# Kernel optimization log

Hardware: AMD Instinct MI355X
Metric: run time of the kernel (lower is better)

The kernel has to match this reference:

```python
import jax, jax.numpy as jnp
import numpy as np

D = 120000   # sample_size
H1 = 600     # sample_size/200
H2 = 300     # sample_size/400
H3 = 200     # sample_size/600
DENSITY = 0.1  # sparselinear default connectivity
B = 512
EPS = 1e-5

_LAYER_SPECS = [(H1, D), (H1, H1), (H2, H1), (H3, H2), (H3, H3)]


def _make_idx(key, out_d, in_d, nnz):
    k1, k2 = jax.random.split(key)
    rows = jax.random.randint(k1, (nnz,), 0, out_d)
    cols = jax.random.randint(k2, (nnz,), 0, in_d)
    return jnp.stack([rows, cols]).astype(jnp.int32)


def setup_inputs() -> dict:
    key = jax.random.key(0)
    ks = jax.random.split(key, 32)
    inp = {"x": jax.random.normal(ks[0], (B, D), jnp.float32)}
    for i, (o, ii) in enumerate(_LAYER_SPECS, 1):
        nnz = int(DENSITY * o * ii)
        scale = 1.0 / np.sqrt(DENSITY * ii)  # kaiming-like fan-in scaling on nonzeros
        inp[f"idx{i}"] = _make_idx(ks[3 * i], o, ii, nnz)
        inp[f"val{i}"] = jax.random.normal(ks[3 * i + 1], (nnz,), jnp.float32) * scale
        inp[f"b{i}"] = jnp.zeros((o,), jnp.float32)
    for j, d in enumerate([H1, H2, H3], 1):
        inp[f"g{j}"] = jnp.ones((d,), jnp.float32)
        inp[f"be{j}"] = jnp.zeros((d,), jnp.float32)
    return inp


def _sp_linear(x, idx, vals, bias, out_d):
    # COO sparse linear: y = x @ W^T + b, W scattered from (row, col, val)
    in_d = x.shape[1]
    W = jnp.zeros((out_d, in_d), x.dtype).at[idx[0], idx[1]].add(vals)
    return x @ W.T + bias


def _bn(x, g, b):
    # BatchNorm1d, training mode: biased batch variance
    m = x.mean(axis=0)
    v = x.var(axis=0)
    return (x - m) * jax.lax.rsqrt(v + EPS) * g + b


def reference(x, idx1, val1, b1, idx2, val2, b2, idx3, val3, b3,
              idx4, val4, b4, idx5, val5, b5,
              g1, be1, g2, be2, g3, be3):
    h = jax.nn.silu(_bn(_sp_linear(x, idx1, val1, b1, H1), g1, be1))
    h = jax.nn.silu(_sp_linear(h, idx2, val2, b2, H1))
    h = jax.nn.silu(_bn(_sp_linear(h, idx3, val3, b3, H2), g2, be2))
    h = jax.nn.silu(_bn(_sp_linear(h, idx4, val4, b4, H3), g3, be3))
    return _sp_linear(h, idx5, val5, b5, H3)
```

## Files before the change

kernel.cpp:

```cpp
#include <hip/hip_runtime.h>

typedef unsigned short ushort_t;
typedef unsigned int uint_t;

typedef __bf16 bf16x8 __attribute__((ext_vector_type(8)));
typedef float  floatx4 __attribute__((ext_vector_type(4)));

#define AS3 __attribute__((address_space(3)))
#define AS1 __attribute__((address_space(1)))

#define BATCH 512
#define D_IN  120000
#define N1P   640
#define N2P   640
#define N3P   320
#define N4P   256
#define N5P   256

#define KSPLIT 50
#define KCHUNK 2400

#define HALF    60000
#define CHW     15000
#define NREG    1200
#define NB      256
#define RSTRIDE 6912

static constexpr long O_W1 = 0;
static constexpr long SZ_W1 = 640L * 120000 * 2;
static constexpr long O_W2 = O_W1 + SZ_W1;
static constexpr long SZ_W2 = 640L * 640 * 4;
static constexpr long O_W3 = O_W2 + SZ_W2;
static constexpr long SZ_W3 = 320L * 640 * 4;
static constexpr long O_W4 = O_W3 + SZ_W3;
static constexpr long SZ_W4 = 256L * 320 * 4;
static constexpr long O_W5 = O_W4 + SZ_W4;
static constexpr long SZ_W5 = 256L * 256 * 4;
static constexpr long O_Y1 = O_W5 + SZ_W5;
static constexpr long SZ_Y1 = 512L * 640 * 4;
static constexpr long ZERO_OFF = O_W2;
static constexpr long ZERO_BYTES = (O_Y1 + SZ_Y1) - O_W2;
static constexpr long O_SCR = O_Y1 + SZ_Y1;
static constexpr long O_CNT = O_SCR;
static constexpr long O_OFF = O_CNT + (long)NREG * NB * 4;
static constexpr long O_TOT = O_OFF + (long)NB * NREG * 4;
static constexpr long O_REC = O_TOT + 4800;
static constexpr long O_H1 = O_SCR;
static constexpr long O_H2 = O_H1 + 512L * 640 * 4;
static constexpr long O_Y3 = O_H2 + 512L * 640 * 4;
static constexpr long O_H3 = O_Y3 + 512L * 320 * 4;
static constexpr long O_Y4 = O_H3 + 512L * 320 * 4;
static constexpr long O_H4 = O_Y4 + 512L * 256 * 4;

__device__ __forceinline__ ushort_t f2bf(float f) {
    union { float f; uint_t u; } x;
    x.f = f;
    uint_t u = x.u;
    return (ushort_t)((u + 0x7FFFu + ((u >> 16) & 1u)) >> 16);
}
__device__ __forceinline__ uint_t cvt_pk_bf16(float lo, float hi) {
    uint_t r;
    asm("v_cvt_pk_bf16_f32 %0, %1, %2" : "=v"(r) : "v"(lo), "v"(hi));
    return r;
}
__device__ __forceinline__ float silu_f(float z) {
    return z / (1.f + expf(-z));
}
__device__ __forceinline__ void load16_lds(const void* g, void* l) {
    __builtin_amdgcn_global_load_lds((const AS1 char*)g, (AS3 char*)l, 16, 0, 0);
}

__global__ void zero_f4(float4* __restrict__ p, long n4) {
    long stride = (long)gridDim.x * blockDim.x;
    for (long i = (long)blockIdx.x * blockDim.x + threadIdx.x; i < n4; i += stride)
        p[i] = make_float4(0.f, 0.f, 0.f, 0.f);
}

__global__ __launch_bounds__(512) void hist1(const int* __restrict__ idx, int nnz, int chunk,
                                             int* __restrict__ counts ) {
    __shared__ uint_t h[NREG];
    const int b = blockIdx.x, t = threadIdx.x;
    for (int i = t; i < NREG; i += 512) h[i] = 0;
    __syncthreads();
    const int s = b * chunk;
    const int e = min(s + chunk, nnz);
    for (int i = s + t; i < e; i += 512) {
        int r = idx[i];
        int c = idx[nnz + i];
        atomicAdd(&h[r * 2 + (c >= HALF ? 1 : 0)], 1u);
    }
    __syncthreads();
    for (int i = t; i < NREG; i += 512) counts[(long)i * NB + b] = (int)h[i];
}

__global__ __launch_bounds__(NB) void scan1(const int* __restrict__ counts ,
                                            int* __restrict__ offs ,
                                            int* __restrict__ totals) {
    __shared__ int s[NB];
    const int reg = blockIdx.x, t = threadIdx.x;
    const int v = counts[(long)reg * NB + t];
    s[t] = v;
    __syncthreads();
    for (int o = 1; o < NB; o <<= 1) {
        int x = (t >= o) ? s[t - o] : 0;
        __syncthreads();
        s[t] += x;
        __syncthreads();
    }
    offs[(long)t * NREG + reg] = s[t] - v;
    if (t == NB - 1) totals[reg] = s[t];
}

__global__ __launch_bounds__(512) void scatter1(const int* __restrict__ idx,
                                                const float* __restrict__ vals,
                                                int nnz, int chunk,
                                                const int* __restrict__ offs ,
                                                int2* __restrict__ rec) {
    __shared__ int cur[NREG];
    const int b = blockIdx.x, t = threadIdx.x;
    const int* ob = offs + (long)b * NREG;
    for (int i = t; i < NREG; i += 512) cur[i] = i * RSTRIDE + ob[i];
    __syncthreads();
    const int s = b * chunk;
    const int e = min(s + chunk, nnz);
    for (int i = s + t; i < e; i += 512) {
        int r = idx[i];
        int c = idx[nnz + i];
        float v = vals[i];
        int h = (c >= HALF) ? 1 : 0;
        int reg = r * 2 + h;
        int slot = atomicAdd(&cur[reg], 1);
        if (slot < (reg + 1) * RSTRIDE)
            rec[slot] = make_int2(c - h * HALF, __float_as_int(v));
    }
}

__global__ __launch_bounds__(512) void build_w1(const int2* __restrict__ rec,
                                                const int* __restrict__ totals,
                                                ushort_t* __restrict__ W) {
    const int bid = blockIdx.x;
    const int r = bid >> 1, h = bid & 1;
    const int t = threadIdx.x;
    ushort_t* dstbase = W + (size_t)r * D_IN + h * HALF;

    if (r >= 600) {
        uint4 z = make_uint4(0, 0, 0, 0);
        for (int j = t * 8; j < HALF; j += 512 * 8) *(uint4*)(dstbase + j) = z;
        return;
    }

    __shared__ int2 lrec[RSTRIDE];
    __shared__ float acc[CHW];

    const int reg = r * 2 + h;
    const int n = min(totals[reg], RSTRIDE);
    const int2* src = rec + (long)reg * RSTRIDE;
    for (int i = t; i < n; i += 512) lrec[i] = src[i];
    __syncthreads();

#pragma unroll
    for (int ch = 0; ch < 4; ch++) {
        for (int j = t * 4; j < CHW; j += 512 * 4)
            *(float4*)&acc[j] = make_float4(0.f, 0.f, 0.f, 0.f);
        __syncthreads();
        const int base = ch * CHW;
        for (int i = t; i < n; i += 512) {
            int2 e = lrec[i];
            unsigned off = (unsigned)(e.x - base);
            if (off < (unsigned)CHW)
                atomicAdd(&acc[off], __int_as_float(e.y));
        }
        __syncthreads();
        ushort_t* dst = dstbase + base;
        for (int j = t * 8; j < CHW; j += 512 * 8) {
            union { ushort_t us[8]; uint4 v; } u;
#pragma unroll
            for (int k = 0; k < 8; k++) u.us[k] = f2bf(acc[j + k]);
            *(uint4*)(dst + j) = u.v;
        }
        __syncthreads();
    }
}

__global__ void scatter_f32(const int* __restrict__ idx, const float* __restrict__ vals,
                            int nnz, float* __restrict__ W, int ldw) {
    int i = blockIdx.x * blockDim.x + threadIdx.x;
    if (i >= nnz) return;
    atomicAdd(&W[(size_t)idx[i] * ldw + idx[nnz + i]], vals[i]);
}

__global__ __launch_bounds__(256) void gemm1(const float* __restrict__ X,
                                             const ushort_t* __restrict__ W,
                                             float* __restrict__ Y) {
    __shared__ ushort_t sA[2][128 * 32];
    __shared__ ushort_t sB[2][128 * 32];

    const int tile = blockIdx.x;
    const int bm = tile / 5, bn = tile % 5;
    const int ks = blockIdx.y * KCHUNK;
    const int iters = KCHUNK / 32;

    const int t = threadIdx.x;
    const int lane = t & 63;
    const int w = t >> 6;
    const int wm = w >> 1, wn = w & 1;
    const int i16 = lane & 15;
    const int qk = lane >> 4;

    const int row0 = t >> 2;
    const int kq = (t & 3) ^ ((t >> 3) & 3);

    const float* pa0 = X + (size_t)(bm * 128 + row0) * D_IN + ks + kq * 8;
    const float* pa1 = pa0 + (size_t)64 * D_IN;
    const ushort_t* pb0 = W + (size_t)(bn * 128 + row0) * D_IN + ks + kq * 8;
    const ushort_t* pb1 = pb0 + (size_t)64 * D_IN;

    int aoff[4], boff[4];
#pragma unroll
    for (int mi = 0; mi < 4; mi++) {
        int row = wm * 64 + mi * 16 + i16;
        aoff[mi] = row * 64 + ((qk ^ ((row >> 1) & 3)) * 16);
    }
#pragma unroll
    for (int ni = 0; ni < 4; ni++) {
        int row = wn * 64 + ni * 16 + i16;
        boff[ni] = row * 64 + ((qk ^ ((row >> 1) & 3)) * 16);
    }
    const char* sAb = (const char*)sA;
    const char* sBb = (const char*)sB;

    floatx4 acc[4][4] = {};

    {
        load16_lds(pb0, &sB[0][(w * 64) * 8]);
        load16_lds(pb1, &sB[0][(256 + w * 64) * 8]);
        float4 a0 = *(const float4*)pa0;
        float4 a1 = *(const float4*)(pa0 + 4);
        float4 a2 = *(const float4*)pa1;
        float4 a3 = *(const float4*)(pa1 + 4);
        uint4 u0, u1;
        u0.x = cvt_pk_bf16(a0.x, a0.y); u0.y = cvt_pk_bf16(a0.z, a0.w);
        u0.z = cvt_pk_bf16(a1.x, a1.y); u0.w = cvt_pk_bf16(a1.z, a1.w);
        u1.x = cvt_pk_bf16(a2.x, a2.y); u1.y = cvt_pk_bf16(a2.z, a2.w);
        u1.z = cvt_pk_bf16(a3.x, a3.y); u1.w = cvt_pk_bf16(a3.z, a3.w);
        *(uint4*)&sA[0][t * 8] = u0;
        *(uint4*)&sA[0][(t + 256) * 8] = u1;
        pa0 += 32; pa1 += 32; pb0 += 32; pb1 += 32;
    }
    __syncthreads();

    int cur = 0;
    for (int it = 0; it < iters; ++it) {
        const int nxt = cur ^ 1;
        const bool pf = (it + 1 < iters);
        float4 a0, a1, a2, a3;
        if (pf) {
            load16_lds(pb0, &sB[nxt][(w * 64) * 8]);
            load16_lds(pb1, &sB[nxt][(256 + w * 64) * 8]);
            a0 = *(const float4*)pa0;
            a1 = *(const float4*)(pa0 + 4);
            a2 = *(const float4*)pa1;
            a3 = *(const float4*)(pa1 + 4);
            pa0 += 32; pa1 += 32; pb0 += 32; pb1 += 32;
        }

        bf16x8 af[4], bfr[4];
#pragma unroll
        for (int mi = 0; mi < 4; mi++)
            af[mi] = *(const bf16x8*)(sAb + cur * 8192 + aoff[mi]);
#pragma unroll
        for (int ni = 0; ni < 4; ni++)
            bfr[ni] = *(const bf16x8*)(sBb + cur * 8192 + boff[ni]);
#pragma unroll
        for (int mi = 0; mi < 4; mi++)
#pragma unroll
            for (int ni = 0; ni < 4; ni++)
                acc[mi][ni] = __builtin_amdgcn_mfma_f32_16x16x32_bf16(af[mi], bfr[ni], acc[mi][ni], 0, 0, 0);

        if (pf) {
            uint4 u0, u1;
            u0.x = cvt_pk_bf16(a0.x, a0.y); u0.y = cvt_pk_bf16(a0.z, a0.w);
            u0.z = cvt_pk_bf16(a1.x, a1.y); u0.w = cvt_pk_bf16(a1.z, a1.w);
            u1.x = cvt_pk_bf16(a2.x, a2.y); u1.y = cvt_pk_bf16(a2.z, a2.w);
            u1.z = cvt_pk_bf16(a3.x, a3.y); u1.w = cvt_pk_bf16(a3.z, a3.w);
            *(uint4*)&sA[nxt][t * 8] = u0;
            *(uint4*)&sA[nxt][(t + 256) * 8] = u1;
        }
        __syncthreads();
        cur = nxt;
    }

#pragma unroll
    for (int mi = 0; mi < 4; mi++) {
#pragma unroll
        for (int ni = 0; ni < 4; ni++) {
#pragma unroll
            for (int r = 0; r < 4; r++) {
                int row = bm * 128 + wm * 64 + mi * 16 + qk * 4 + r;
                int col = bn * 128 + wn * 64 + ni * 16 + i16;
                atomicAdd(&Y[(size_t)row * N1P + col], acc[mi][ni][r]);
            }
        }
    }
}

__global__ __launch_bounds__(512) void bn_silu(const float* __restrict__ Y, int ld, int realN,
                                               const float* __restrict__ g,
                                               const float* __restrict__ be,
                                               float* __restrict__ H) {
    const int t = threadIdx.x;
    const int sub = t >> 6;
    const int c = t & 63;
    const int col = blockIdx.x * 64 + c;

    float s = 0.f, ss = 0.f;
#pragma unroll 8
    for (int r = sub; r < BATCH; r += 8) {
        float v = Y[(size_t)r * ld + col];
        s += v;
        ss += v * v;
    }
    __shared__ float rs[8][64], rq[8][64], scs[64], shs[64];
    rs[sub][c] = s;
    rq[sub][c] = ss;
    __syncthreads();
    if (t < 64) {
        float S = 0.f, SS = 0.f;
#pragma unroll
        for (int k = 0; k < 8; k++) { S += rs[k][t]; SS += rq[k][t]; }
        float mean = S * (1.f / 512.f);
        float var  = SS * (1.f / 512.f) - mean * mean;
        int cc = blockIdx.x * 64 + t;
        float sc = 0.f, sh = 0.f;
        if (cc < realN) {
            sc = rsqrtf(var + 1e-5f) * g[cc];
            sh = be[cc] - mean * sc;
        }
        scs[t] = sc;
        shs[t] = sh;
    }
    __syncthreads();
    const float sc = scs[c], sh = shs[c];
#pragma unroll 8
    for (int r = sub; r < BATCH; r += 8) {
        float v = Y[(size_t)r * ld + col];
        H[(size_t)r * ld + col] = silu_f(v * sc + sh);
    }
}

template <int ACT, int GUARD>
__global__ __launch_bounds__(256) void small_gemm(const float* __restrict__ A, int lda,
                                                  const float* __restrict__ W, int ldw,
                                                  const float* __restrict__ bias, int biasN,
                                                  float* __restrict__ out, int ldo, int outN,
                                                  int K) {
    __shared__ float sA[64][20];
    __shared__ float sB[64][20];
    const int t = threadIdx.x;
    const int m0 = blockIdx.x * 64, n0 = blockIdx.y * 64;
    const int ty = t >> 4, tx = t & 15;
    const int lm = t >> 2, lq = t & 3;
    float acc[4][4] = {};

    for (int kt = 0; kt < K; kt += 16) {
        __syncthreads();
        float4 av = *(const float4*)&A[(size_t)(m0 + lm) * lda + kt + lq * 4];
        float4 wv = *(const float4*)&W[(size_t)(n0 + lm) * ldw + kt + lq * 4];
        sA[lm][lq * 4 + 0] = av.x; sA[lm][lq * 4 + 1] = av.y;
        sA[lm][lq * 4 + 2] = av.z; sA[lm][lq * 4 + 3] = av.w;
        sB[lm][lq * 4 + 0] = wv.x; sB[lm][lq * 4 + 1] = wv.y;
        sB[lm][lq * 4 + 2] = wv.z; sB[lm][lq * 4 + 3] = wv.w;
        __syncthreads();
#pragma unroll
        for (int kg = 0; kg < 4; kg++) {
            float4 a4[4], b4[4];
#pragma unroll
            for (int i = 0; i < 4; i++) a4[i] = *(const float4*)&sA[ty * 4 + i][kg * 4];
#pragma unroll
            for (int j = 0; j < 4; j++) b4[j] = *(const float4*)&sB[tx * 4 + j][kg * 4];
#pragma unroll
            for (int i = 0; i < 4; i++)
#pragma unroll
                for (int j = 0; j < 4; j++)
                    acc[i][j] += a4[i].x * b4[j].x + a4[i].y * b4[j].y +
                                 a4[i].z * b4[j].z + a4[i].w * b4[j].w;
        }
    }

#pragma unroll
    for (int i = 0; i < 4; i++) {
#pragma unroll
        for (int j = 0; j < 4; j++) {
            int row = m0 + ty * 4 + i;
            int col = n0 + tx * 4 + j;
            float v = acc[i][j];
            if (bias != nullptr && col < biasN) v += bias[col];
            if (ACT == 1) v = silu_f(v);
            if (GUARD) {
                if (col < outN) out[(size_t)row * ldo + col] = v;
            } else {
                out[(size_t)row * ldo + col] = v;
            }
        }
    }
}

extern "C" void kernel_launch(void* const* d_in, const int* in_sizes, int n_in,
                              void* d_out, int out_size, void* d_ws, size_t ws_size,
                              hipStream_t stream) {
    const float* x   = (const float*)d_in[0];
    const int* idx1 = (const int*)d_in[1];  const float* val1 = (const float*)d_in[2];
    const int* idx2 = (const int*)d_in[4];  const float* val2 = (const float*)d_in[5];
    const float* b2 = (const float*)d_in[6];
    const int* idx3 = (const int*)d_in[7];  const float* val3 = (const float*)d_in[8];
    const int* idx4 = (const int*)d_in[10]; const float* val4 = (const float*)d_in[11];
    const int* idx5 = (const int*)d_in[13]; const float* val5 = (const float*)d_in[14];
    const float* b5 = (const float*)d_in[15];
    const float* g1 = (const float*)d_in[16]; const float* be1 = (const float*)d_in[17];
    const float* g2 = (const float*)d_in[18]; const float* be2 = (const float*)d_in[19];
    const float* g3 = (const float*)d_in[20]; const float* be3 = (const float*)d_in[21];

    const int nnz1 = in_sizes[1] / 2;
    const int nnz2 = in_sizes[4] / 2;
    const int nnz3 = in_sizes[7] / 2;
    const int nnz4 = in_sizes[10] / 2;
    const int nnz5 = in_sizes[13] / 2;

    char* ws = (char*)d_ws;
    ushort_t* W1 = (ushort_t*)(ws + O_W1);
    float* W2 = (float*)(ws + O_W2);
    float* W3 = (float*)(ws + O_W3);
    float* W4 = (float*)(ws + O_W4);
    float* W5 = (float*)(ws + O_W5);
    float* y1 = (float*)(ws + O_Y1);
    int*   cnt = (int*)(ws + O_CNT);
    int*   off = (int*)(ws + O_OFF);
    int*   tot = (int*)(ws + O_TOT);
    int2*  rec = (int2*)(ws + O_REC);
    float* h1 = (float*)(ws + O_H1);
    float* h2 = (float*)(ws + O_H2);
    float* y3 = (float*)(ws + O_Y3);
    float* h3 = (float*)(ws + O_H3);
    float* y4 = (float*)(ws + O_Y4);
    float* h4 = (float*)(ws + O_H4);

    zero_f4<<<dim3((unsigned)(ZERO_BYTES / 16 / 256 + 1)), dim3(256), 0, stream>>>(
        (float4*)(ws + ZERO_OFF), ZERO_BYTES / 16);

    {
        const int chunk = (nnz1 + NB - 1) / NB;
        hist1<<<dim3(NB), dim3(512), 0, stream>>>(idx1, nnz1, chunk, cnt);
        scan1<<<dim3(NREG), dim3(NB), 0, stream>>>(cnt, off, tot);
        scatter1<<<dim3(NB), dim3(512), 0, stream>>>(idx1, val1, nnz1, chunk, off, rec);
        build_w1<<<dim3(640 * 2), dim3(512), 0, stream>>>(rec, tot, W1);
    }

    scatter_f32<<<dim3((nnz2 + 255) / 256), dim3(256), 0, stream>>>(idx2, val2, nnz2, W2, 640);
    scatter_f32<<<dim3((nnz3 + 255) / 256), dim3(256), 0, stream>>>(idx3, val3, nnz3, W3, 640);
    scatter_f32<<<dim3((nnz4 + 255) / 256), dim3(256), 0, stream>>>(idx4, val4, nnz4, W4, 320);
    scatter_f32<<<dim3((nnz5 + 255) / 256), dim3(256), 0, stream>>>(idx5, val5, nnz5, W5, 256);

    gemm1<<<dim3(20, KSPLIT), dim3(256), 0, stream>>>(x, W1, y1);

    bn_silu<<<dim3(N1P / 64), dim3(512), 0, stream>>>(y1, N1P, 600, g1, be1, h1);

    small_gemm<1, 0><<<dim3(8, N2P / 64), dim3(256), 0, stream>>>(h1, N1P, W2, 640, b2, 600,
                                                                  h2, N2P, N2P, 640);
    small_gemm<0, 0><<<dim3(8, N3P / 64), dim3(256), 0, stream>>>(h2, N2P, W3, 640, nullptr, 0,
                                                                  y3, N3P, N3P, 640);
    bn_silu<<<dim3(N3P / 64), dim3(512), 0, stream>>>(y3, N3P, 300, g2, be2, h3);

    small_gemm<0, 0><<<dim3(8, N4P / 64), dim3(256), 0, stream>>>(h3, N3P, W4, 320, nullptr, 0,
                                                                  y4, N4P, N4P, 320);
    bn_silu<<<dim3(N4P / 64), dim3(512), 0, stream>>>(y4, N4P, 200, g3, be3, h4);

    small_gemm<0, 1><<<dim3(8, N5P / 64), dim3(256), 0, stream>>>(h4, N4P, W5, 256, b5, 200,
                                                                  (float*)d_out, 200, 200, 256);
    (void)n_in; (void)out_size; (void)ws_size;
}
```

Measured before the change: 1.113 ms.

## Pre-cast X to bf16 and load gemm1 A tiles directly into LDS

A new kernel converts the whole f32 input X to bf16 in workspace before gemm1. gemm1 can then stream both A and B tiles with global_load_lds, dropping the register staging and in-loop conversion of A. The grid is also flattened and remapped so consecutive blocks on each XCD share the same K-chunk, aiming for better L2 reuse of X and W1 across the 20 output tiles. The cost is an extra full read of X plus a write and re-read of the bf16 copy. The bf16 buffer also reuses workspace regions that earlier kernels use for histogram and scatter data.

```diff
diff --git a/kernel.cpp b/kernel.cpp
--- a/kernel.cpp
+++ b/kernel.cpp
@@ -40,12 +40,13 @@
 static constexpr long SZ_Y1 = 512L * 640 * 4;
 static constexpr long ZERO_OFF = O_W2;
 static constexpr long ZERO_BYTES = (O_Y1 + SZ_Y1) - O_W2;
-static constexpr long O_SCR = O_Y1 + SZ_Y1;
-static constexpr long O_CNT = O_SCR;
+static constexpr long O_XB = O_Y1 + SZ_Y1;
+static constexpr long SZ_XB = 512L * 120000 * 2;
+static constexpr long O_CNT = O_XB;
 static constexpr long O_OFF = O_CNT + (long)NREG * NB * 4;
 static constexpr long O_TOT = O_OFF + (long)NB * NREG * 4;
 static constexpr long O_REC = O_TOT + 4800;
-static constexpr long O_H1 = O_SCR;
+static constexpr long O_H1 = O_XB;
 static constexpr long O_H2 = O_H1 + 512L * 640 * 4;
 static constexpr long O_Y3 = O_H2 + 512L * 640 * 4;
 static constexpr long O_H3 = O_Y3 + 512L * 320 * 4;
@@ -58,11 +59,6 @@
     uint_t u = x.u;
     return (ushort_t)((u + 0x7FFFu + ((u >> 16) & 1u)) >> 16);
 }
-__device__ __forceinline__ uint_t cvt_pk_bf16(float lo, float hi) {
-    uint_t r;
-    asm("v_cvt_pk_bf16_f32 %0, %1, %2" : "=v"(r) : "v"(lo), "v"(hi));
-    return r;
-}
 __device__ __forceinline__ float silu_f(float z) {
     return z / (1.f + expf(-z));
 }
@@ -74,6 +70,17 @@
     long stride = (long)gridDim.x * blockDim.x;
     for (long i = (long)blockIdx.x * blockDim.x + threadIdx.x; i < n4; i += stride)
         p[i] = make_float4(0.f, 0.f, 0.f, 0.f);
+}
+
+__global__ void cast_f32_bf16(const float* __restrict__ X, ushort_t* __restrict__ Xb, long n8) {
+    long t = (long)blockIdx.x * blockDim.x + threadIdx.x;
+    if (t >= n8) return;
+    const float4* p = (const float4*)X + 2 * t;
+    float4 a = p[0], b = p[1];
+    union { ushort_t us[8]; uint4 v; } u;
+    u.us[0] = f2bf(a.x); u.us[1] = f2bf(a.y); u.us[2] = f2bf(a.z); u.us[3] = f2bf(a.w);
+    u.us[4] = f2bf(b.x); u.us[5] = f2bf(b.y); u.us[6] = f2bf(b.z); u.us[7] = f2bf(b.w);
+    ((uint4*)Xb)[t] = u.v;
 }
 
 __global__ __launch_bounds__(512) void hist1(const int* __restrict__ idx, int nnz, int chunk,
@@ -189,15 +196,18 @@
     atomicAdd(&W[(size_t)idx[i] * ldw + idx[nnz + i]], vals[i]);
 }
 
-__global__ __launch_bounds__(256) void gemm1(const float* __restrict__ X,
+__global__ __launch_bounds__(256) void gemm1(const ushort_t* __restrict__ X,
                                              const ushort_t* __restrict__ W,
                                              float* __restrict__ Y) {
     __shared__ ushort_t sA[2][128 * 32];
     __shared__ ushort_t sB[2][128 * 32];
 
-    const int tile = blockIdx.x;
+    const int b = blockIdx.x;
+    const int wrk = (b & 7) * 125 + (b >> 3);
+    const int ksIdx = wrk / 20;
+    const int tile = wrk % 20;
     const int bm = tile / 5, bn = tile % 5;
-    const int ks = blockIdx.y * KCHUNK;
+    const int ks = ksIdx * KCHUNK;
     const int iters = KCHUNK / 32;
 
     const int t = threadIdx.x;
@@ -210,8 +220,8 @@
     const int row0 = t >> 2;
     const int kq = (t & 3) ^ ((t >> 3) & 3);
 
-    const float* pa0 = X + (size_t)(bm * 128 + row0) * D_IN + ks + kq * 8;
-    const float* pa1 = pa0 + (size_t)64 * D_IN;
+    const ushort_t* pa0 = X + (size_t)(bm * 128 + row0) * D_IN + ks + kq * 8;
+    const ushort_t* pa1 = pa0 + (size_t)64 * D_IN;
     const ushort_t* pb0 = W + (size_t)(bn * 128 + row0) * D_IN + ks + kq * 8;
     const ushort_t* pb1 = pb0 + (size_t)64 * D_IN;
 
@@ -231,36 +241,21 @@
 
     floatx4 acc[4][4] = {};
 
-    {
-        load16_lds(pb0, &sB[0][(w * 64) * 8]);
-        load16_lds(pb1, &sB[0][(256 + w * 64) * 8]);
-        float4 a0 = *(const float4*)pa0;
-        float4 a1 = *(const float4*)(pa0 + 4);
-        float4 a2 = *(const float4*)pa1;
-        float4 a3 = *(const float4*)(pa1 + 4);
-        uint4 u0, u1;
-        u0.x = cvt_pk_bf16(a0.x, a0.y); u0.y = cvt_pk_bf16(a0.z, a0.w);
-        u0.z = cvt_pk_bf16(a1.x, a1.y); u0.w = cvt_pk_bf16(a1.z, a1.w);
-        u1.x = cvt_pk_bf16(a2.x, a2.y); u1.y = cvt_pk_bf16(a2.z, a2.w);
-        u1.z = cvt_pk_bf16(a3.x, a3.y); u1.w = cvt_pk_bf16(a3.z, a3.w);
-        *(uint4*)&sA[0][t * 8] = u0;
-        *(uint4*)&sA[0][(t + 256) * 8] = u1;
-        pa0 += 32; pa1 += 32; pb0 += 32; pb1 += 32;
-    }
+    load16_lds(pa0, &sA[0][(w * 64) * 8]);
+    load16_lds(pa1, &sA[0][(256 + w * 64) * 8]);
+    load16_lds(pb0, &sB[0][(w * 64) * 8]);
+    load16_lds(pb1, &sB[0][(256 + w * 64) * 8]);
+    pa0 += 32; pa1 += 32; pb0 += 32; pb1 += 32;
     __syncthreads();
 
     int cur = 0;
     for (int it = 0; it < iters; ++it) {
         const int nxt = cur ^ 1;
-        const bool pf = (it + 1 < iters);
-        float4 a0, a1, a2, a3;
-        if (pf) {
+        if (it + 1 < iters) {
+            load16_lds(pa0, &sA[nxt][(w * 64) * 8]);
+            load16_lds(pa1, &sA[nxt][(256 + w * 64) * 8]);
             load16_lds(pb0, &sB[nxt][(w * 64) * 8]);
             load16_lds(pb1, &sB[nxt][(256 + w * 64) * 8]);
-            a0 = *(const float4*)pa0;
-            a1 = *(const float4*)(pa0 + 4);
-            a2 = *(const float4*)pa1;
-            a3 = *(const float4*)(pa1 + 4);
             pa0 += 32; pa1 += 32; pb0 += 32; pb1 += 32;
         }
 
@@ -277,15 +272,6 @@
             for (int ni = 0; ni < 4; ni++)
                 acc[mi][ni] = __builtin_amdgcn_mfma_f32_16x16x32_bf16(af[mi], bfr[ni], acc[mi][ni], 0, 0, 0);
 
-        if (pf) {
-            uint4 u0, u1;
-            u0.x = cvt_pk_bf16(a0.x, a0.y); u0.y = cvt_pk_bf16(a0.z, a0.w);
-            u0.z = cvt_pk_bf16(a1.x, a1.y); u0.w = cvt_pk_bf16(a1.z, a1.w);
-            u1.x = cvt_pk_bf16(a2.x, a2.y); u1.y = cvt_pk_bf16(a2.z, a2.w);
-            u1.z = cvt_pk_bf16(a3.x, a3.y); u1.w = cvt_pk_bf16(a3.z, a3.w);
-            *(uint4*)&sA[nxt][t * 8] = u0;
-            *(uint4*)&sA[nxt][(t + 256) * 8] = u1;
-        }
         __syncthreads();
         cur = nxt;
     }
@@ -437,6 +423,7 @@
     int*   off = (int*)(ws + O_OFF);
     int*   tot = (int*)(ws + O_TOT);
     int2*  rec = (int2*)(ws + O_REC);
+    ushort_t* Xb = (ushort_t*)(ws + O_XB);
     float* h1 = (float*)(ws + O_H1);
     float* h2 = (float*)(ws + O_H2);
     float* y3 = (float*)(ws + O_Y3);
@@ -455,12 +442,17 @@
         build_w1<<<dim3(640 * 2), dim3(512), 0, stream>>>(rec, tot, W1);
     }
 
+    {
+        long n8 = (long)BATCH * D_IN / 8;
+        cast_f32_bf16<<<dim3((unsigned)((n8 + 255) / 256)), dim3(256), 0, stream>>>(x, Xb, n8);
+    }
+
     scatter_f32<<<dim3((nnz2 + 255) / 256), dim3(256), 0, stream>>>(idx2, val2, nnz2, W2, 640);
     scatter_f32<<<dim3((nnz3 + 255) / 256), dim3(256), 0, stream>>>(idx3, val3, nnz3, W3, 640);
     scatter_f32<<<dim3((nnz4 + 255) / 256), dim3(256), 0, stream>>>(idx4, val4, nnz4, W4, 320);
     scatter_f32<<<dim3((nnz5 + 255) / 256), dim3(256), 0, stream>>>(idx5, val5, nnz5, W5, 256);
 
-    gemm1<<<dim3(20, KSPLIT), dim3(256), 0, stream>>>(x, W1, y1);
+    gemm1<<<dim3(8 * 125), dim3(256), 0, stream>>>(Xb, W1, y1);
 
     bn_silu<<<dim3(N1P / 64), dim3(512), 0, stream>>>(y1, N1P, 600, g1, be1, h1);
 
```

Measured after the change: 1.078 ms. 3.2% less time.
